# Performance work log

Measured on AMD Instinct MI355X. Metric: run time of the kernel, lower is better.

The kernel has to match this reference:

```python
import jax, jax.numpy as jnp
import numpy as np

DEPTH = 8
DIM = 1024
DI = 2 * DIM        # d_inner (expand=2)
DSTATE = 16         # d_state
DCONV = 4           # conv kernel width
DTRANK = DIM // 16  # dt_rank = ceil(d_model/16) = 64
B = 2
L = 2048
EPS = 1e-5


def setup_inputs() -> dict:
    key = jax.random.key(0)
    ks = jax.random.split(key, 8)
    s = 0.02
    A_log = jnp.broadcast_to(
        jnp.log(jnp.arange(1, DSTATE + 1, dtype=jnp.float32)), (DEPTH, DI, DSTATE)
    )
    return {
        "x": jax.random.normal(ks[0], (B, L, DIM), jnp.float32),
        "in_proj_w": jax.random.normal(ks[1], (DEPTH, 2 * DI, DIM), jnp.float32) * s,
        "conv_w": jax.random.normal(ks[2], (DEPTH, DI, DCONV), jnp.float32) * s,
        "conv_b": jnp.zeros((DEPTH, DI), jnp.float32),
        "x_proj_w": jax.random.normal(ks[3], (DEPTH, DTRANK + 2 * DSTATE, DI), jnp.float32) * s,
        "dt_proj_w": jax.random.normal(ks[4], (DEPTH, DI, DTRANK), jnp.float32) * s,
        "dt_proj_b": jax.random.normal(ks[5], (DEPTH, DI), jnp.float32) * 0.1,
        "A_log": A_log + 0.0,
        "D": jnp.ones((DEPTH, DI), jnp.float32),
        "out_proj_w": jax.random.normal(ks[6], (DEPTH, DIM, DI), jnp.float32) * s,
        "rms_w": jnp.ones((DEPTH, DIM), jnp.float32),
    }


def _selective_scan(xs, delta, Bm, Cm, A):
    # xs, delta: [B, L, DI]; Bm, Cm: [B, L, DSTATE]; A: [DI, DSTATE]
    def step(h, t):
        dt, Bt, Ct, xt = t  # [B,DI], [B,N], [B,N], [B,DI]
        dA = jnp.exp(dt[:, :, None] * A)                      # [B,DI,N]
        h = dA * h + (dt * xt)[:, :, None] * Bt[:, None, :]   # [B,DI,N]
        y = jnp.einsum('bdn,bn->bd', h, Ct)                   # [B,DI]
        return h, y

    h0 = jnp.zeros((xs.shape[0], xs.shape[2], A.shape[1]), xs.dtype)
    ts = (delta.transpose(1, 0, 2), Bm.transpose(1, 0, 2),
          Cm.transpose(1, 0, 2), xs.transpose(1, 0, 2))
    _, ys = jax.lax.scan(step, h0, ts)  # ys: [L,B,DI]
    return ys.transpose(1, 0, 2)


def _mamba(x, Wi, cw, cb, Wx, Wdt, bdt, A_log, Dp, Wo):
    # in_proj (no bias): [B,L,DIM] -> [B,L,2*DI]
    xz = jnp.einsum('bld,ed->ble', x, Wi)
    xs, z = jnp.split(xz, 2, axis=-1)
    # depthwise causal conv1d, kernel DCONV, left pad DCONV-1
    xc = jax.lax.conv_general_dilated(
        xs.transpose(0, 2, 1), cw[:, None, :], (1,), [(DCONV - 1, 0)],
        dimension_numbers=('NCH', 'OIH', 'NCH'), feature_group_count=DI)
    xs = jax.nn.silu(xc + cb[None, :, None]).transpose(0, 2, 1)  # [B,L,DI]
    # x_proj -> dt, B, C
    xdbl = jnp.einsum('bld,ed->ble', xs, Wx)
    dt, Bm, Cm = jnp.split(xdbl, [DTRANK, DTRANK + DSTATE], axis=-1)
    delta = jax.nn.softplus(jnp.einsum('blr,dr->bld', dt, Wdt) + bdt)  # [B,L,DI]
    A = -jnp.exp(A_log)  # [DI, DSTATE]
    y = _selective_scan(xs, delta, Bm, Cm, A) + xs * Dp
    y = y * jax.nn.silu(z)
    return jnp.einsum('bld,ed->ble', y, Wo)  # out_proj, no bias


def _rmsnorm(x, w):
    return x * jax.lax.rsqrt(jnp.mean(x * x, axis=-1, keepdims=True) + EPS) * w


def reference(x, in_proj_w, conv_w, conv_b, x_proj_w, dt_proj_w, dt_proj_b,
              A_log, D, out_proj_w, rms_w):
    for i in range(DEPTH):
        x = _mamba(x, in_proj_w[i], conv_w[i], conv_b[i], x_proj_w[i],
                   dt_proj_w[i], dt_proj_b[i], A_log[i], D[i], out_proj_w[i])
        x = _rmsnorm(x, rms_w[i])
    return x
```

## Files before the change

### kernel.cpp

```cpp
#include <hip/hip_runtime.h>
#include <cstddef>

#define DEPTH  8
#define DIMM   1024
#define DI     2048
#define NST    16
#define DCONVK 4
#define DTRANK 64
#define BB     2
#define LL     2048
#define MM     (BB*LL)
#define BD     (BB*DI)
#define CHK    32
#define LC     (LL/CHK)
#define LOG2E  1.44269504088896f

typedef __attribute__((ext_vector_type(8))) short bf16x8;
typedef __attribute__((ext_vector_type(4))) float f32x4;

__device__ __forceinline__ unsigned short f2bf(float f) {
  unsigned int u = __float_as_uint(f);
  unsigned int r = (u + 0x7fffu + ((u >> 16) & 1u)) >> 16;
  return (unsigned short)r;
}
__device__ __forceinline__ float bf2f(unsigned short h) {
  return __uint_as_float(((unsigned int)h) << 16);
}

__global__ __launch_bounds__(256) void cvt2_k(const float* __restrict__ x,
                                              unsigned short* __restrict__ p,
                                              size_t n) {
  size_t i = ((size_t)blockIdx.x * 256 + threadIdx.x) * 4;
  float4 v = *(const float4*)(x + i);
  float vv[4] = {v.x, v.y, v.z, v.w};
  unsigned short u1[4], u2[4];
#pragma unroll
  for (int k = 0; k < 4; ++k) {
    unsigned short h1 = f2bf(vv[k]);
    u1[k] = h1;
    u2[k] = f2bf(vv[k] - bf2f(h1));
  }
  *(ushort4*)(p + i)     = make_ushort4(u1[0], u1[1], u1[2], u1[3]);
  *(ushort4*)(p + n + i) = make_ushort4(u2[0], u2[1], u2[2], u2[3]);
}

template <int TM>
__global__ __launch_bounds__(256) void gemm_mp(
    const unsigned short* __restrict__ Ap, int lda_a, int pstr_a,
    const unsigned short* __restrict__ Bp, int lda_b, int pstr_b,
    float* __restrict__ C, int M, int N, int K) {
  constexpr int NP    = 2;
  constexpr int NSLOT = NP * (TM + 128) * 4;
  constexpr int ITERS = NSLOT / 256;
  constexpr int NF    = (TM == 128) ? 4 : 2;
  __shared__ unsigned short S[NP * (TM + 128) * 32];

  const int t   = threadIdx.x;
  const int w   = t >> 6;
  const int l   = t & 63;
  const int lm  = l & 15;
  const int q8  = (l >> 4) << 3;
  const int qs  = q8 ^ (((lm >> 1) & 3) << 3);
  const int m0  = blockIdx.y * TM;
  const int n0  = blockIdx.x * 128;
  const int wm  = (TM == 128) ? ((w & 1) << 6) : 0;
  const int wn  = (TM == 128) ? ((w >> 1) << 6) : (w << 5);

  const unsigned short* src[ITERS];
  unsigned short* dst[ITERS];
#pragma unroll
  for (int it = 0; it < ITERS; ++it) {
    int c = it * 256 + t;
    const unsigned short* base;
    int r, aslot;
    if (c < NP * TM * 4) {
      int p  = c / (TM * 4);
      int wi = c % (TM * 4);
      r = wi >> 2; aslot = wi & 3;
      base = Ap + (size_t)p * pstr_a + (size_t)(m0 + r) * lda_a;
    } else {
      int c2 = c - NP * TM * 4;
      int p  = c2 >> 9;
      int wi = c2 & 511;
      r = wi >> 2; aslot = wi & 3;
      base = Bp + (size_t)p * pstr_b + (size_t)(n0 + r) * lda_b;
    }
    int kq = (aslot ^ ((r >> 1) & 3)) << 3;
    src[it] = base + kq;
    dst[it] = &S[(size_t)(it * 256 + (w << 6)) * 8];
  }

  f32x4 acc[4][NF];
#pragma unroll
  for (int i = 0; i < 4; ++i)
#pragma unroll
    for (int j = 0; j < NF; ++j) acc[i][j] = (f32x4){0.f, 0.f, 0.f, 0.f};

  for (int k0 = 0; k0 < K; k0 += 32) {
#pragma unroll
    for (int it = 0; it < ITERS; ++it) {
      __builtin_amdgcn_global_load_lds(
          (const __attribute__((address_space(1))) unsigned int*)src[it],
          (__attribute__((address_space(3))) unsigned int*)dst[it], 16, 0, 0);
      src[it] += 32;
    }
    __syncthreads();
    bf16x8 a0[4], aX[4], b0[NF];
#pragma unroll
    for (int i = 0; i < 4; ++i)
      a0[i] = *(const bf16x8*)&S[(wm + i * 16 + lm) * 32 + qs];
#pragma unroll
    for (int j = 0; j < NF; ++j)
      b0[j] = *(const bf16x8*)&S[NP * TM * 32 + (wn + j * 16 + lm) * 32 + qs];
#pragma unroll
    for (int i = 0; i < 4; ++i)
#pragma unroll
      for (int j = 0; j < NF; ++j)
        acc[i][j] = __builtin_amdgcn_mfma_f32_16x16x32_bf16(a0[i], b0[j], acc[i][j], 0, 0, 0);
#pragma unroll
    for (int j = 0; j < NF; ++j)
      aX[j & 3] = *(const bf16x8*)&S[NP * TM * 32 + 128 * 32 + (wn + j * 16 + lm) * 32 + qs];
#pragma unroll
    for (int i = 0; i < 4; ++i)
#pragma unroll
      for (int j = 0; j < NF; ++j)
        acc[i][j] = __builtin_amdgcn_mfma_f32_16x16x32_bf16(a0[i], aX[j], acc[i][j], 0, 0, 0);
#pragma unroll
    for (int i = 0; i < 4; ++i)
      aX[i] = *(const bf16x8*)&S[TM * 32 + (wm + i * 16 + lm) * 32 + qs];
#pragma unroll
    for (int i = 0; i < 4; ++i)
#pragma unroll
      for (int j = 0; j < NF; ++j)
        acc[i][j] = __builtin_amdgcn_mfma_f32_16x16x32_bf16(aX[i], b0[j], acc[i][j], 0, 0, 0);
    __syncthreads();
  }

  const int row0 = (l >> 4) << 2;
#pragma unroll
  for (int i = 0; i < 4; ++i)
#pragma unroll
    for (int j = 0; j < NF; ++j)
#pragma unroll
      for (int r = 0; r < 4; ++r) {
        int m = m0 + wm + i * 16 + row0 + r;
        int n = n0 + wn + j * 16 + lm;
        C[(size_t)m * N + n] = acc[i][j][r];
      }
}

__global__ __launch_bounds__(256) void dtproj_mp(const unsigned short* __restrict__ Ap,
                                                 const unsigned short* __restrict__ Bp,
                                                 const float* __restrict__ bdt,
                                                 float* __restrict__ Cd) {
  __shared__ unsigned short S[32768];
  const int t  = threadIdx.x;
  const int w  = t >> 6;
  const int l  = t & 63;
  const int lm = l & 15;
  const int q8 = (l >> 4) << 3;
  const int qs = q8 ^ (((lm >> 1) & 3) << 3);
  const int m0 = blockIdx.y * 128;
  const int n0 = blockIdx.x * 128;
  const int wm = (w & 1) << 6;
  const int wn = (w >> 1) << 6;

#pragma unroll
  for (int it = 0; it < 16; ++it) {
    int c  = it * 256 + t;
    int kt = c >> 11;
    int c2 = c & 2047;
    const unsigned short* base;
    int r, aslot;
    if (c2 < 1024) {
      int p = c2 >> 9; int wi = c2 & 511; r = wi >> 2; aslot = wi & 3;
      base = Ap + (size_t)p * (MM * 64) + (size_t)(m0 + r) * 64;
    } else {
      int c3 = c2 - 1024;
      int p = c3 >> 9; int wi = c3 & 511; r = wi >> 2; aslot = wi & 3;
      base = Bp + (size_t)p * (DI * 64) + (size_t)(n0 + r) * 64;
    }
    int kq = (aslot ^ ((r >> 1) & 3)) << 3;
    __builtin_amdgcn_global_load_lds(
        (const __attribute__((address_space(1))) unsigned int*)(base + kt * 32 + kq),
        (__attribute__((address_space(3))) unsigned int*)&S[(size_t)(it * 256 + (w << 6)) * 8],
        16, 0, 0);
  }
  __syncthreads();

  f32x4 acc[4][4];
#pragma unroll
  for (int i = 0; i < 4; ++i)
#pragma unroll
    for (int j = 0; j < 4; ++j) acc[i][j] = (f32x4){0.f, 0.f, 0.f, 0.f};

#pragma unroll
  for (int kt = 0; kt < 2; ++kt) {
    const int RA = kt * 16384;
    const int RB = kt * 16384 + 8192;
    bf16x8 a0[4], aX[4], b0[4];
#pragma unroll
    for (int i = 0; i < 4; ++i)
      a0[i] = *(const bf16x8*)&S[RA + (wm + i * 16 + lm) * 32 + qs];
#pragma unroll
    for (int j = 0; j < 4; ++j)
      b0[j] = *(const bf16x8*)&S[RB + (wn + j * 16 + lm) * 32 + qs];
#pragma unroll
    for (int i = 0; i < 4; ++i)
#pragma unroll
      for (int j = 0; j < 4; ++j)
        acc[i][j] = __builtin_amdgcn_mfma_f32_16x16x32_bf16(a0[i], b0[j], acc[i][j], 0, 0, 0);
#pragma unroll
    for (int j = 0; j < 4; ++j)
      aX[j] = *(const bf16x8*)&S[RB + 4096 + (wn + j * 16 + lm) * 32 + qs];
#pragma unroll
    for (int i = 0; i < 4; ++i)
#pragma unroll
      for (int j = 0; j < 4; ++j)
        acc[i][j] = __builtin_amdgcn_mfma_f32_16x16x32_bf16(a0[i], aX[j], acc[i][j], 0, 0, 0);
#pragma unroll
    for (int i = 0; i < 4; ++i)
      aX[i] = *(const bf16x8*)&S[RA + 4096 + (wm + i * 16 + lm) * 32 + qs];
#pragma unroll
    for (int i = 0; i < 4; ++i)
#pragma unroll
      for (int j = 0; j < 4; ++j)
        acc[i][j] = __builtin_amdgcn_mfma_f32_16x16x32_bf16(aX[i], b0[j], acc[i][j], 0, 0, 0);
  }

  const int row0 = (l >> 4) << 2;
#pragma unroll
  for (int j = 0; j < 4; ++j) {
    int n = n0 + wn + j * 16 + lm;
    float bv = bdt[n];
#pragma unroll
    for (int i = 0; i < 4; ++i)
#pragma unroll
      for (int r = 0; r < 4; ++r) {
        int m = m0 + wm + i * 16 + row0 + r;
        float x = acc[i][j][r] + bv;
        Cd[(size_t)m * DI + n] = fmaxf(x, 0.f) + log1pf(expf(-fabsf(x)));
      }
  }
}

#define XPN 96
__global__ __launch_bounds__(256) void xproj_part_k(const float* __restrict__ A,
                                                    const float* __restrict__ W,
                                                    float* __restrict__ Cp) {
  __shared__ float As[16][128];
  __shared__ float Ws[16][XPN];
  const int t  = threadIdx.x;
  const int tx = t & 15;
  const int ty = t >> 4;
  const int m0 = blockIdx.x * 128;
  const int kb = blockIdx.y * 256;
  float acc[8][6];
#pragma unroll
  for (int i = 0; i < 8; ++i)
#pragma unroll
    for (int j = 0; j < 6; ++j) acc[i][j] = 0.f;

  for (int k0 = kb; k0 < kb + 256; k0 += 16) {
#pragma unroll
    for (int e = t; e < 512; e += 256) {
      int r = e >> 2, cq = (e & 3) << 2;
      float4 v = *(const float4*)(A + (size_t)(m0 + r) * DI + k0 + cq);
      As[cq+0][r] = v.x; As[cq+1][r] = v.y; As[cq+2][r] = v.z; As[cq+3][r] = v.w;
    }
    for (int e = t; e < 384; e += 256) {
      int r = e >> 2, cq = (e & 3) << 2;
      float4 v = *(const float4*)(W + (size_t)r * DI + k0 + cq);
      Ws[cq+0][r] = v.x; Ws[cq+1][r] = v.y; Ws[cq+2][r] = v.z; Ws[cq+3][r] = v.w;
    }
    __syncthreads();
#pragma unroll
    for (int kk = 0; kk < 16; ++kk) {
      float a[8], b[6];
#pragma unroll
      for (int i = 0; i < 8; ++i) a[i] = As[kk][ty*8 + i];
#pragma unroll
      for (int j = 0; j < 6; ++j) b[j] = Ws[kk][tx*6 + j];
#pragma unroll
      for (int i = 0; i < 8; ++i)
#pragma unroll
        for (int j = 0; j < 6; ++j) acc[i][j] += a[i] * b[j];
    }
    __syncthreads();
  }
  float* cp = Cp + (size_t)blockIdx.y * MM * XPN;
#pragma unroll
  for (int i = 0; i < 8; ++i)
#pragma unroll
    for (int j = 0; j < 6; ++j)
      cp[(size_t)(m0 + ty*8 + i) * XPN + tx*6 + j] = acc[i][j];
}

__global__ __launch_bounds__(256) void xproj_red_k(const float* __restrict__ Cp,
                                                   float* __restrict__ o,
                                                   unsigned short* __restrict__ dtp) {
  int i = blockIdx.x * 256 + threadIdx.x;
  float s = 0.f;
#pragma unroll
  for (int ks = 0; ks < 8; ++ks) s += Cp[(size_t)ks * (MM * XPN) + i];
  o[i] = s;
  int m = i / 96, col = i - m * 96;
  if (col < DTRANK) {
    unsigned short h1 = f2bf(s);
    dtp[(size_t)m * DTRANK + col] = h1;
    dtp[(size_t)MM * DTRANK + (size_t)m * DTRANK + col] = f2bf(s - bf2f(h1));
  }
}

__device__ __forceinline__ float fast_silu(float x) {
  return x * __builtin_amdgcn_rcpf(1.f + exp2f(-LOG2E * x));
}

__global__ __launch_bounds__(256) void conv_silu_k(const float* __restrict__ xz,
                                                   const float* __restrict__ cw,
                                                   const float* __restrict__ cb,
                                                   float* __restrict__ xc) {
  int idx = blockIdx.x * 256 + threadIdx.x;
  int c  = idx & (DI - 1);
  int bl = idx >> 11;
  int l  = bl & (LL - 1);
  float acc = cb[c];
#pragma unroll
  for (int k = 0; k < DCONVK; ++k) {
    int ls = l - (DCONVK - 1) + k;
    if (ls >= 0)
      acc += xz[(size_t)(bl - (DCONVK - 1) + k) * (2*DI) + c] * cw[c*DCONVK + k];
  }
  xc[idx] = fast_silu(acc);
}

__global__ __launch_bounds__(256) void scan_pass1(const float* __restrict__ delta,
                                                  const float* __restrict__ xc,
                                                  const float* __restrict__ xdbl,
                                                  const float* __restrict__ A_log,
                                                  float* __restrict__ Hc,
                                                  float* __restrict__ Sdt) {
  const int t  = threadIdx.x;
  const int c  = blockIdx.x >> 6;
  const int g  = blockIdx.x & 63;
  const int q  = t >> 2;
  const int nq = t & 3;
  const int ch = g * 64 + q;
  const int b  = ch >> 11;
  const int d  = ch & (DI - 1);
  const size_t rowbase = (size_t)b * LL + (size_t)c * LC;

  __shared__ float Bs[LC * 16];
  { int row = t >> 2, seg = t & 3;
    *(float4*)&Bs[row * 16 + seg * 4] =
        *(const float4*)(xdbl + (rowbase + row) * 96 + DTRANK + seg * 4);
  }
  __syncthreads();

  float4 al = *(const float4*)(A_log + (size_t)d * NST + nq * 4);
  const float Av0 = -expf(al.x) * LOG2E, Av1 = -expf(al.y) * LOG2E;
  const float Av2_ = -expf(al.z) * LOG2E, Av3 = -expf(al.w) * LOG2E;
  float h0 = 0.f, h1 = 0.f, h2 = 0.f, h3 = 0.f, S = 0.f;

#define P1_SU 4
  float aD[P1_SU], aX[P1_SU];
  float bD[P1_SU], bX[P1_SU];

#define P1_LOAD(l0, D_, X_)                                            \
  { _Pragma("unroll")                                                  \
    for (int u = 0; u < P1_SU; ++u) {                                  \
      size_t bl = rowbase + (l0) + u;                                  \
      D_[u] = delta[bl * DI + d];                                      \
      X_[u] = xc[bl * DI + d];                                         \
    } }

#define P1_COMP(l0, D_, X_)                                            \
  { _Pragma("unroll")                                                  \
    for (int u = 0; u < P1_SU; ++u) {                                  \
      float4 Bv = *(const float4*)&Bs[((l0) + u) * 16 + nq * 4];       \
      float dt = D_[u], uB = dt * X_[u];                               \
      h0 = fmaf(exp2f(dt * Av0), h0, uB * Bv.x);                       \
      h1 = fmaf(exp2f(dt * Av1), h1, uB * Bv.y);                       \
      h2 = fmaf(exp2f(dt * Av2_), h2, uB * Bv.z);                      \
      h3 = fmaf(exp2f(dt * Av3), h3, uB * Bv.w);                       \
      S += dt;                                                         \
    } }

  P1_LOAD(0, aD, aX);
  for (int l0 = 0; l0 < LC; l0 += 2 * P1_SU) {
    P1_LOAD(l0 + P1_SU, bD, bX);
    P1_COMP(l0, aD, aX);
    if (l0 + 2 * P1_SU < LC) P1_LOAD(l0 + 2 * P1_SU, aD, aX);
    P1_COMP(l0 + P1_SU, bD, bX);
  }
#undef P1_LOAD
#undef P1_COMP
  size_t hi = ((size_t)c * BD + ch) * NST + nq * 4;
  float4 hv; hv.x = h0; hv.y = h1; hv.z = h2; hv.w = h3;
  *(float4*)(Hc + hi) = hv;
  if (nq == 0) Sdt[(size_t)c * BD + ch] = S;
}

__global__ __launch_bounds__(256) void scan_pass2(float* __restrict__ Hc,
                                                  const float* __restrict__ Sdt,
                                                  const float* __restrict__ A_log) {
  const int g  = blockIdx.x * 256 + threadIdx.x;
  const int n  = g & (NST - 1);
  const int ch = g >> 4;
  const int d  = ch & (DI - 1);
  const float Av2 = -expf(A_log[d * NST + n]) * LOG2E;
  float Sv[CHK];
#pragma unroll
  for (int c = 0; c < CHK; ++c) Sv[c] = Sdt[(size_t)c * BD + ch];
  float h = 0.f;
  float tmp = Hc[(size_t)ch * NST + n];
#pragma unroll
  for (int c = 0; c < CHK; ++c) {
    size_t idx = ((size_t)c * BD + ch) * NST + n;
    float tnext = (c + 1 < CHK) ? Hc[((size_t)(c+1) * BD + ch) * NST + n] : 0.f;
    Hc[idx] = h;
    h = fmaf(exp2f(Av2 * Sv[c]), h, tmp);
    tmp = tnext;
  }
}

__global__ __launch_bounds__(256) void scan_pass3(const float* __restrict__ delta,
                                                  const float* __restrict__ xc,
                                                  const float* __restrict__ xdbl,
                                                  const float* __restrict__ A_log,
                                                  float* __restrict__ xzp,
                                                  const float* __restrict__ Dp,
                                                  const float* __restrict__ Hc) {
  const int t  = threadIdx.x;
  const int c  = blockIdx.x >> 6;
  const int g  = blockIdx.x & 63;
  const int q  = t >> 2;
  const int nq = t & 3;
  const int ch = g * 64 + q;
  const int b  = ch >> 11;
  const int d  = ch & (DI - 1);
  const size_t rowbase = (size_t)b * LL + (size_t)c * LC;

  __shared__ float BCs[LC * 32];
  {
#pragma unroll
    for (int e = t; e < 512; e += 256) {
      int row = e >> 3, seg = e & 7;
      *(float4*)&BCs[row * 32 + seg * 4] =
          *(const float4*)(xdbl + (rowbase + row) * 96 + DTRANK + seg * 4);
    }
  }
  __syncthreads();

  float4 al = *(const float4*)(A_log + (size_t)d * NST + nq * 4);
  const float Av0 = -expf(al.x) * LOG2E, Av1 = -expf(al.y) * LOG2E;
  const float Av2_ = -expf(al.z) * LOG2E, Av3 = -expf(al.w) * LOG2E;
  const float Dv = Dp[d];
  float4 hv = *(const float4*)(Hc + ((size_t)c * BD + ch) * NST + nq * 4);
  float h0 = hv.x, h1 = hv.y, h2 = hv.z, h3 = hv.w;
  unsigned short* yp = (unsigned short*)xzp;

#define P3_SU 2
  float aD[P3_SU], aX[P3_SU], aZ[P3_SU];
  float bD[P3_SU], bX[P3_SU], bZ[P3_SU];

#define P3_LOAD(l0, D_, X_, Z_)                                        \
  { _Pragma("unroll")                                                  \
    for (int u = 0; u < P3_SU; ++u) {                                  \
      size_t bl = rowbase + (l0) + u;                                  \
      D_[u] = delta[bl * DI + d];                                      \
      X_[u] = xc[bl * DI + d];                                         \
      Z_[u] = xzp[bl * (2*DI) + DI + d];                               \
    } }

#define P3_COMP(l0, D_, X_, Z_)                                        \
  { _Pragma("unroll")                                                  \
    for (int u = 0; u < P3_SU; ++u) {                                  \
      float4 Bv = *(const float4*)&BCs[((l0) + u) * 32 + nq * 4];      \
      float4 Cv = *(const float4*)&BCs[((l0) + u) * 32 + 16 + nq * 4]; \
      float dt = D_[u], uB = dt * X_[u];                               \
      h0 = fmaf(exp2f(dt * Av0), h0, uB * Bv.x);                       \
      h1 = fmaf(exp2f(dt * Av1), h1, uB * Bv.y);                       \
      h2 = fmaf(exp2f(dt * Av2_), h2, uB * Bv.z);                      \
      h3 = fmaf(exp2f(dt * Av3), h3, uB * Bv.w);                       \
      float s = fmaf(h1, Cv.y, h0 * Cv.x);                             \
      float t2 = fmaf(h3, Cv.w, h2 * Cv.z);                            \
      s += t2;                                                         \
      s += __shfl_xor(s, 1, 4);                                        \
      s += __shfl_xor(s, 2, 4);                                        \
      if (nq == 0) {                                                   \
        float yv = (s + X_[u] * Dv) * fast_silu(Z_[u]);                \
        unsigned short y1 = f2bf(yv);                                  \
        unsigned short y2 = f2bf(yv - bf2f(y1));                       \
        size_t bl = rowbase + (l0) + u;                                \
        yp[bl * 8192 + d] = y1;                                        \
        yp[bl * 8192 + 2048 + d] = y2;                                 \
      }                                                                \
    } }

  P3_LOAD(0, aD, aX, aZ);
  for (int l0 = 0; l0 < LC; l0 += 2 * P3_SU) {
    P3_LOAD(l0 + P3_SU, bD, bX, bZ);
    P3_COMP(l0, aD, aX, aZ);
    if (l0 + 2 * P3_SU < LC) P3_LOAD(l0 + 2 * P3_SU, aD, aX, aZ);
    P3_COMP(l0 + P3_SU, bD, bX, bZ);
  }
#undef P3_LOAD
#undef P3_COMP
}

template <bool PLANES>
__global__ __launch_bounds__(256) void rmsnorm_k(const float* __restrict__ x,
                                                 const float* __restrict__ w,
                                                 float* __restrict__ o,
                                                 unsigned short* __restrict__ op) {
  int row = blockIdx.x;
  const float* xr = x + (size_t)row * DIMM;
  float s = 0.f;
  for (int i = threadIdx.x; i < DIMM; i += 256) { float v = xr[i]; s += v * v; }
#pragma unroll
  for (int off = 32; off > 0; off >>= 1) s += __shfl_xor(s, off, 64);
  __shared__ float red[4];
  if ((threadIdx.x & 63) == 0) red[threadIdx.x >> 6] = s;
  __syncthreads();
  float tot = red[0] + red[1] + red[2] + red[3];
  float scale = rsqrtf(tot * (1.0f / DIMM) + 1e-5f);
  for (int i = threadIdx.x; i < DIMM; i += 256) {
    float v = xr[i] * scale * w[i];
    if (PLANES) {
      unsigned short h1 = f2bf(v);
      op[(size_t)row * DIMM + i] = h1;
      op[(size_t)MM * DIMM + (size_t)row * DIMM + i] = f2bf(v - bf2f(h1));
    } else {
      o[(size_t)row * DIMM + i] = v;
    }
  }
}

extern "C" void kernel_launch(void* const* d_in, const int* in_sizes, int n_in,
                              void* d_out, int out_size, void* d_ws, size_t ws_size,
                              hipStream_t stream) {
  (void)in_sizes; (void)n_in; (void)out_size; (void)ws_size;
  const float* x_in    = (const float*)d_in[0];
  const float* Wi_all  = (const float*)d_in[1];
  const float* cw_all  = (const float*)d_in[2];
  const float* cb_all  = (const float*)d_in[3];
  const float* Wx_all  = (const float*)d_in[4];
  const float* Wdt_all = (const float*)d_in[5];
  const float* bdt_all = (const float*)d_in[6];
  const float* Alog_all= (const float*)d_in[7];
  const float* D_all   = (const float*)d_in[8];
  const float* Wo_all  = (const float*)d_in[9];
  const float* rw_all  = (const float*)d_in[10];
  float* out = (float*)d_out;

  float* ws    = (float*)d_ws;
  float* xz    = ws;
  float* xc    = xz   + (size_t)MM * 2 * DI;
  float* xdbl  = xc   + (size_t)MM * DI;
  float* delta = xdbl + (size_t)MM * 96;
  float* xbuf  = delta+ (size_t)MM * DI;
  float* outtmp = xc;

  unsigned short* xpl  = (unsigned short*)delta;
  unsigned short* wipl = (unsigned short*)xc;
  unsigned short* wopl = (unsigned short*)(xc + (size_t)4194304);
  float*          Cp   = delta;
  float* Hc   = xbuf;
  float* Sdt  = Hc + (size_t)CHK * BD * NST;
  unsigned short* dtpl  = (unsigned short*)(xbuf + 2228224);
  unsigned short* wdtpl = (unsigned short*)(xbuf + 2490368);

  const int EW_GRID = (MM * DI) / 256;
  const int SCAN_GRID = CHK * 64;

  for (int i = 0; i < DEPTH; ++i) {
    const float* Wi   = Wi_all  + (size_t)i * (2*DI) * DIMM;
    const float* cw   = cw_all  + (size_t)i * DI * DCONVK;
    const float* cb   = cb_all  + (size_t)i * DI;
    const float* Wx   = Wx_all  + (size_t)i * 96 * DI;
    const float* Wdt  = Wdt_all + (size_t)i * DI * DTRANK;
    const float* bdt  = bdt_all + (size_t)i * DI;
    const float* Alog = Alog_all+ (size_t)i * DI * NST;
    const float* Dp   = D_all   + (size_t)i * DI;
    const float* Wo   = Wo_all  + (size_t)i * DIMM * DI;
    const float* rw   = rw_all  + (size_t)i * DIMM;

    if (i == 0)
      cvt2_k<<<(MM*DIMM)/1024, 256, 0, stream>>>(x_in, xpl, (size_t)MM * DIMM);
    cvt2_k<<<((2*DI)*DIMM)/1024, 256, 0, stream>>>(Wi, wipl, (size_t)(2*DI) * DIMM);
    gemm_mp<128><<<dim3((2*DI)/128, MM/128), 256, 0, stream>>>(
        xpl, DIMM, MM*DIMM, wipl, DIMM, (2*DI)*DIMM, xz, MM, 2*DI, DIMM);
    conv_silu_k<<<EW_GRID, 256, 0, stream>>>(xz, cw, cb, xc);
    xproj_part_k<<<dim3(MM/128, 8), 256, 0, stream>>>(xc, Wx, Cp);
    xproj_red_k<<<(MM*XPN)/256, 256, 0, stream>>>(Cp, xdbl, dtpl);
    cvt2_k<<<(DI*DTRANK)/1024, 256, 0, stream>>>(Wdt, wdtpl, (size_t)DI * DTRANK);
    dtproj_mp<<<dim3(DI/128, MM/128), 256, 0, stream>>>(dtpl, wdtpl, bdt, delta);
    scan_pass1<<<SCAN_GRID, 256, 0, stream>>>(delta, xc, xdbl, Alog, Hc, Sdt);
    scan_pass2<<<(BD*NST)/256, 256, 0, stream>>>(Hc, Sdt, Alog);
    scan_pass3<<<SCAN_GRID, 256, 0, stream>>>(delta, xc, xdbl, Alog, xz, Dp, Hc);
    cvt2_k<<<(DIMM*DI)/1024, 256, 0, stream>>>(Wo, wopl, (size_t)DIMM * DI);
    gemm_mp<64><<<dim3(DIMM/128, MM/64), 256, 0, stream>>>(
        (const unsigned short*)xz, 8192, 2048, wopl, DI, DIMM*DI,
        outtmp, MM, DIMM, DI);
    if (i < DEPTH - 1)
      rmsnorm_k<true><<<MM, 256, 0, stream>>>(outtmp, rw, nullptr, xpl);
    else
      rmsnorm_k<false><<<MM, 256, 0, stream>>>(outtmp, rw, out, nullptr);
  }
}
```

Before: 3.663 ms.

## Add 256x256-tile in_proj GEMM with async LDS loads and split-phase pipelining

```diff
diff --git a/kernel.cpp b/kernel.cpp
--- a/kernel.cpp
+++ b/kernel.cpp
@@ -141,6 +141,129 @@
   for (int i = 0; i < 4; ++i)
 #pragma unroll
     for (int j = 0; j < NF; ++j)
+#pragma unroll
+      for (int r = 0; r < 4; ++r) {
+        int m = m0 + wm + i * 16 + row0 + r;
+        int n = n0 + wn + j * 16 + lm;
+        C[(size_t)m * N + n] = acc[i][j][r];
+      }
+}
+
+__global__ __launch_bounds__(512) void gemm256_mp(
+    const unsigned short* __restrict__ Ap, int lda_a, int pstr_a,
+    const unsigned short* __restrict__ Bp, int lda_b, int pstr_b,
+    float* __restrict__ C, int M, int N, int K) {
+  __shared__ unsigned short S[65536];
+  const int t  = threadIdx.x;
+  const int w  = t >> 6;
+  const int l  = t & 63;
+  const int lm = l & 15;
+  const int qs = ((l >> 4) << 3) ^ (((lm >> 1) & 3) << 3);
+  const int m0 = blockIdx.y * 256;
+  const int n0 = blockIdx.x * 256;
+  const int wm = (w & 1) << 7;
+  const int wn = (w >> 1) << 6;
+
+  const int rr = t >> 2;
+  const int kq = ((t & 3) ^ ((rr >> 1) & 3)) << 3;
+  const unsigned short* srcA = Ap + (size_t)(m0 + rr) * lda_a + kq;
+  const unsigned short* srcB = Bp + (size_t)(n0 + rr) * lda_b + kq;
+  const size_t a128 = (size_t)128 * lda_a;
+  const size_t b128 = (size_t)128 * lda_b;
+  const int dbase = (w << 6) * 8;
+
+#define G256_ISSUE(p_, it_)                                                    \
+  __builtin_amdgcn_global_load_lds(                                            \
+      (const __attribute__((address_space(1))) unsigned int*)(p_),             \
+      (__attribute__((address_space(3))) unsigned int*)&S[bnext + (it_)*4096 + dbase], \
+      16, 0, 0)
+
+  f32x4 acc[8][4];
+#pragma unroll
+  for (int i = 0; i < 8; ++i)
+#pragma unroll
+    for (int j = 0; j < 4; ++j) acc[i][j] = (f32x4){0.f, 0.f, 0.f, 0.f};
+
+  {
+    const int bnext = 0;
+    const size_t kb = 0;
+    G256_ISSUE(srcA + kb, 0);          G256_ISSUE(srcA + a128 + kb, 1);
+    G256_ISSUE(srcB + kb, 4);          G256_ISSUE(srcB + b128 + kb, 5);
+    G256_ISSUE(srcB + pstr_b + kb, 6); G256_ISSUE(srcB + pstr_b + b128 + kb, 7);
+    G256_ISSUE(srcA + pstr_a + kb, 2); G256_ISSUE(srcA + pstr_a + a128 + kb, 3);
+  }
+  asm volatile("s_waitcnt vmcnt(4)" ::: "memory");
+  __builtin_amdgcn_s_barrier();
+
+  const int NT = K >> 5;
+#pragma unroll 2
+  for (int ti = 0; ti < NT; ++ti) {
+    const int bcur  = (ti & 1) << 15;
+    const int bnext = bcur ^ 32768;
+    const int kkt   = (ti + 1 < NT) ? (ti + 1) : 0;
+    const size_t kb = (size_t)kkt * 32;
+    const unsigned short* Sb = &S[bcur];
+    bf16x8 a[8], b0[4], b1[4];
+
+#pragma unroll
+    for (int i = 0; i < 8; ++i)
+      a[i] = *(const bf16x8*)&Sb[(wm + i * 16 + lm) * 32 + qs];
+#pragma unroll
+    for (int j = 0; j < 4; ++j)
+      b0[j] = *(const bf16x8*)&Sb[16384 + (wn + j * 16 + lm) * 32 + qs];
+    G256_ISSUE(srcA + kb, 0); G256_ISSUE(srcA + a128 + kb, 1);
+    G256_ISSUE(srcB + kb, 4); G256_ISSUE(srcB + b128 + kb, 5);
+    asm volatile("s_waitcnt vmcnt(6)" ::: "memory");
+    __builtin_amdgcn_s_barrier();
+    asm volatile("s_waitcnt lgkmcnt(0)" ::: "memory");
+    __builtin_amdgcn_s_setprio(1);
+#pragma unroll
+    for (int i = 0; i < 8; ++i)
+#pragma unroll
+      for (int j = 0; j < 4; ++j)
+        acc[i][j] = __builtin_amdgcn_mfma_f32_16x16x32_bf16(a[i], b0[j], acc[i][j], 0, 0, 0);
+    __builtin_amdgcn_s_setprio(0);
+    __builtin_amdgcn_s_barrier();
+
+#pragma unroll
+    for (int j = 0; j < 4; ++j)
+      b1[j] = *(const bf16x8*)&Sb[24576 + (wn + j * 16 + lm) * 32 + qs];
+    G256_ISSUE(srcB + pstr_b + kb, 6); G256_ISSUE(srcB + pstr_b + b128 + kb, 7);
+    asm volatile("s_waitcnt vmcnt(6)" ::: "memory");
+    __builtin_amdgcn_s_barrier();
+    asm volatile("s_waitcnt lgkmcnt(0)" ::: "memory");
+    __builtin_amdgcn_s_setprio(1);
+#pragma unroll
+    for (int i = 0; i < 8; ++i)
+#pragma unroll
+      for (int j = 0; j < 4; ++j)
+        acc[i][j] = __builtin_amdgcn_mfma_f32_16x16x32_bf16(a[i], b1[j], acc[i][j], 0, 0, 0);
+    __builtin_amdgcn_s_setprio(0);
+    __builtin_amdgcn_s_barrier();
+
+#pragma unroll
+    for (int i = 0; i < 8; ++i)
+      a[i] = *(const bf16x8*)&Sb[8192 + (wm + i * 16 + lm) * 32 + qs];
+    G256_ISSUE(srcA + pstr_a + kb, 2); G256_ISSUE(srcA + pstr_a + a128 + kb, 3);
+    asm volatile("s_waitcnt vmcnt(4)" ::: "memory");
+    __builtin_amdgcn_s_barrier();
+    asm volatile("s_waitcnt lgkmcnt(0)" ::: "memory");
+    __builtin_amdgcn_s_setprio(1);
+#pragma unroll
+    for (int i = 0; i < 8; ++i)
+#pragma unroll
+      for (int j = 0; j < 4; ++j)
+        acc[i][j] = __builtin_amdgcn_mfma_f32_16x16x32_bf16(a[i], b0[j], acc[i][j], 0, 0, 0);
+    __builtin_amdgcn_s_setprio(0);
+    __builtin_amdgcn_s_barrier();
+  }
+#undef G256_ISSUE
+
+  const int row0 = (l >> 4) << 2;
+#pragma unroll
+  for (int i = 0; i < 8; ++i)
+#pragma unroll
+    for (int j = 0; j < 4; ++j)
 #pragma unroll
       for (int r = 0; r < 4; ++r) {
         int m = m0 + wm + i * 16 + row0 + r;
@@ -589,7 +712,7 @@
     if (i == 0)
       cvt2_k<<<(MM*DIMM)/1024, 256, 0, stream>>>(x_in, xpl, (size_t)MM * DIMM);
     cvt2_k<<<((2*DI)*DIMM)/1024, 256, 0, stream>>>(Wi, wipl, (size_t)(2*DI) * DIMM);
-    gemm_mp<128><<<dim3((2*DI)/128, MM/128), 256, 0, stream>>>(
+    gemm256_mp<<<dim3((2*DI)/256, MM/256), 512, 0, stream>>>(
         xpl, DIMM, MM*DIMM, wipl, DIMM, (2*DI)*DIMM, xz, MM, 2*DI, DIMM);
     conv_silu_k<<<EW_GRID, 256, 0, stream>>>(xz, cw, cb, xc);
     xproj_part_k<<<dim3(MM/128, 8), 256, 0, stream>>>(xc, Wx, Cp);
```

New measurement: 3.356 ms. -8.4%, faster.

## Replace split-bf16 GEMM with 256-row double-buffered two-phase kernel and split-K out_proj

Applied to the files above, without the earlier changes.

```diff
diff --git a/kernel.cpp b/kernel.cpp
--- a/kernel.cpp
+++ b/kernel.cpp
@@ -44,108 +44,145 @@
   *(ushort4*)(p + n + i) = make_ushort4(u2[0], u2[1], u2[2], u2[3]);
 }
 
-template <int TM>
-__global__ __launch_bounds__(256) void gemm_mp(
+template <int BN, int NSPLIT>
+__global__ __launch_bounds__(512, 2) void gemm2ph(
     const unsigned short* __restrict__ Ap, int lda_a, int pstr_a,
     const unsigned short* __restrict__ Bp, int lda_b, int pstr_b,
-    float* __restrict__ C, int M, int N, int K) {
-  constexpr int NP    = 2;
-  constexpr int NSLOT = NP * (TM + 128) * 4;
-  constexpr int ITERS = NSLOT / 256;
-  constexpr int NF    = (TM == 128) ? 4 : 2;
-  __shared__ unsigned short S[NP * (TM + 128) * 32];
-
-  const int t   = threadIdx.x;
-  const int w   = t >> 6;
-  const int l   = t & 63;
-  const int lm  = l & 15;
-  const int q8  = (l >> 4) << 3;
-  const int qs  = q8 ^ (((lm >> 1) & 3) << 3);
-  const int m0  = blockIdx.y * TM;
-  const int n0  = blockIdx.x * 128;
-  const int wm  = (TM == 128) ? ((w & 1) << 6) : 0;
-  const int wn  = (TM == 128) ? ((w >> 1) << 6) : (w << 5);
-
-  const unsigned short* src[ITERS];
-  unsigned short* dst[ITERS];
-#pragma unroll
-  for (int it = 0; it < ITERS; ++it) {
-    int c = it * 256 + t;
-    const unsigned short* base;
-    int r, aslot;
-    if (c < NP * TM * 4) {
-      int p  = c / (TM * 4);
-      int wi = c % (TM * 4);
-      r = wi >> 2; aslot = wi & 3;
-      base = Ap + (size_t)p * pstr_a + (size_t)(m0 + r) * lda_a;
-    } else {
-      int c2 = c - NP * TM * 4;
-      int p  = c2 >> 9;
-      int wi = c2 & 511;
-      r = wi >> 2; aslot = wi & 3;
-      base = Bp + (size_t)p * pstr_b + (size_t)(n0 + r) * lda_b;
-    }
-    int kq = (aslot ^ ((r >> 1) & 3)) << 3;
-    src[it] = base + kq;
-    dst[it] = &S[(size_t)(it * 256 + (w << 6)) * 8];
-  }
-
-  f32x4 acc[4][NF];
-#pragma unroll
-  for (int i = 0; i < 4; ++i)
-#pragma unroll
-    for (int j = 0; j < NF; ++j) acc[i][j] = (f32x4){0.f, 0.f, 0.f, 0.f};
-
-  for (int k0 = 0; k0 < K; k0 += 32) {
-#pragma unroll
-    for (int it = 0; it < ITERS; ++it) {
-      __builtin_amdgcn_global_load_lds(
-          (const __attribute__((address_space(1))) unsigned int*)src[it],
-          (__attribute__((address_space(3))) unsigned int*)dst[it], 16, 0, 0);
-      src[it] += 32;
-    }
-    __syncthreads();
-    bf16x8 a0[4], aX[4], b0[NF];
-#pragma unroll
-    for (int i = 0; i < 4; ++i)
-      a0[i] = *(const bf16x8*)&S[(wm + i * 16 + lm) * 32 + qs];
-#pragma unroll
-    for (int j = 0; j < NF; ++j)
-      b0[j] = *(const bf16x8*)&S[NP * TM * 32 + (wn + j * 16 + lm) * 32 + qs];
-#pragma unroll
-    for (int i = 0; i < 4; ++i)
-#pragma unroll
-      for (int j = 0; j < NF; ++j)
-        acc[i][j] = __builtin_amdgcn_mfma_f32_16x16x32_bf16(a0[i], b0[j], acc[i][j], 0, 0, 0);
-#pragma unroll
-    for (int j = 0; j < NF; ++j)
-      aX[j & 3] = *(const bf16x8*)&S[NP * TM * 32 + 128 * 32 + (wn + j * 16 + lm) * 32 + qs];
-#pragma unroll
-    for (int i = 0; i < 4; ++i)
-#pragma unroll
-      for (int j = 0; j < NF; ++j)
-        acc[i][j] = __builtin_amdgcn_mfma_f32_16x16x32_bf16(a0[i], aX[j], acc[i][j], 0, 0, 0);
-#pragma unroll
-    for (int i = 0; i < 4; ++i)
-      aX[i] = *(const bf16x8*)&S[TM * 32 + (wm + i * 16 + lm) * 32 + qs];
-#pragma unroll
-    for (int i = 0; i < 4; ++i)
-#pragma unroll
-      for (int j = 0; j < NF; ++j)
-        acc[i][j] = __builtin_amdgcn_mfma_f32_16x16x32_bf16(aX[i], b0[j], acc[i][j], 0, 0, 0);
-    __syncthreads();
-  }
-
+    float* __restrict__ C0, float* __restrict__ C1, int N, int Ktot) {
+  constexpr int BM  = 256;
+  constexpr int BF  = BN / 64;
+  constexpr int BL  = BN / 128;
+  constexpr int RA1 = BM * 32;
+  constexpr int RB0 = 2 * BM * 32;
+  constexpr int RB1 = 2 * BM * 32 + BN * 32;
+  constexpr int BUFS = (2 * BM + 2 * BN) * 32;
+  __shared__ unsigned short S[2 * BUFS];
+
+  const int t  = threadIdx.x;
+  const int w  = t >> 6;
+  const int l  = t & 63;
+  const int lm = l & 15;
+  const int qs = ((l >> 4) << 3) ^ (((lm >> 1) & 3) << 3);
+
+  const int nx   = gridDim.x;
+  const int nwg  = nx * gridDim.y;
+  const int flat = blockIdx.y * nx + blockIdx.x;
+  const int swz  = (flat & 7) * (nwg >> 3) + (flat >> 3);
+  const int m0 = (swz / nx) * BM;
+  const int n0 = (swz % nx) * BN;
+  const int z  = (NSPLIT == 2) ? blockIdx.z : 0;
+  const int KS = Ktot / NSPLIT;
+
+  const int wm = (w & 1) << 7;
+  const int wn = (w >> 1) * (BN / 4);
+
+  const int rr = t >> 2;
+  const int kq = ((t & 3) ^ ((rr >> 1) & 3)) << 3;
+  const unsigned short* srcA = Ap + (size_t)(m0 + rr) * lda_a + (size_t)z * KS + kq;
+  const unsigned short* srcB = Bp + (size_t)(n0 + rr) * lda_b + (size_t)z * KS + kq;
+  const size_t a128 = (size_t)128 * lda_a;
+  const size_t b128 = (size_t)128 * lda_b;
+  const int dbase = (w << 6) * 8;
+
+#define GI(p_, off_)                                                           \
+  __builtin_amdgcn_global_load_lds(                                            \
+      (const __attribute__((address_space(1))) unsigned int*)(p_),             \
+      (__attribute__((address_space(3))) unsigned int*)&S[bnext + (off_) + dbase], \
+      16, 0, 0)
+
+#define GI_PH0(kb_)                                                            \
+  { GI(srcA + (kb_), 0); GI(srcA + a128 + (kb_), 4096);                        \
+    GI(srcB + (kb_), RB0);                                                     \
+    if (BL == 2) GI(srcB + b128 + (kb_), RB0 + 4096);                          \
+    GI(srcB + (size_t)pstr_b + (kb_), RB1);                                    \
+    if (BL == 2) GI(srcB + (size_t)pstr_b + b128 + (kb_), RB1 + 4096); }
+
+#define GI_PH1(kb_)                                                            \
+  { GI(srcA + (size_t)pstr_a + (kb_), RA1);                                    \
+    GI(srcA + (size_t)pstr_a + a128 + (kb_), RA1 + 4096); }
+
+  f32x4 acc[8][BF];
+#pragma unroll
+  for (int i = 0; i < 8; ++i)
+#pragma unroll
+    for (int j = 0; j < BF; ++j) acc[i][j] = (f32x4){0.f, 0.f, 0.f, 0.f};
+
+  {
+    const int bnext = 0;
+    GI_PH0((size_t)0);
+    GI_PH1((size_t)0);
+  }
+  asm volatile("s_waitcnt vmcnt(2)" ::: "memory");
+  __builtin_amdgcn_s_barrier();
+
+  const int NT = KS >> 5;
+#pragma unroll 2
+  for (int ti = 0; ti < NT; ++ti) {
+    const int bcur  = (ti & 1) ? BUFS : 0;
+    const int bnext = (ti & 1) ? 0 : BUFS;
+    const size_t kb = (size_t)((ti + 1 < NT) ? (ti + 1) : 0) * 32;
+    const unsigned short* Sb = &S[bcur];
+    bf16x8 a[8], b0[BF], b1[BF];
+
+#pragma unroll
+    for (int i = 0; i < 8; ++i)
+      a[i] = *(const bf16x8*)&Sb[(wm + i * 16 + lm) * 32 + qs];
+#pragma unroll
+    for (int j = 0; j < BF; ++j)
+      b0[j] = *(const bf16x8*)&Sb[RB0 + (wn + j * 16 + lm) * 32 + qs];
+#pragma unroll
+    for (int j = 0; j < BF; ++j)
+      b1[j] = *(const bf16x8*)&Sb[RB1 + (wn + j * 16 + lm) * 32 + qs];
+    GI_PH0(kb);
+    if constexpr (BN == 256) asm volatile("s_waitcnt vmcnt(6)" ::: "memory");
+    else                     asm volatile("s_waitcnt vmcnt(4)" ::: "memory");
+    __builtin_amdgcn_s_barrier();
+    asm volatile("s_waitcnt lgkmcnt(0)" ::: "memory");
+    __builtin_amdgcn_s_setprio(1);
+#pragma unroll
+    for (int i = 0; i < 8; ++i)
+#pragma unroll
+      for (int j = 0; j < BF; ++j)
+        acc[i][j] = __builtin_amdgcn_mfma_f32_16x16x32_bf16(a[i], b0[j], acc[i][j], 0, 0, 0);
+#pragma unroll
+    for (int i = 0; i < 8; ++i)
+#pragma unroll
+      for (int j = 0; j < BF; ++j)
+        acc[i][j] = __builtin_amdgcn_mfma_f32_16x16x32_bf16(a[i], b1[j], acc[i][j], 0, 0, 0);
+    __builtin_amdgcn_s_setprio(0);
+    __builtin_amdgcn_s_barrier();
+
+#pragma unroll
+    for (int i = 0; i < 8; ++i)
+      a[i] = *(const bf16x8*)&Sb[RA1 + (wm + i * 16 + lm) * 32 + qs];
+    GI_PH1(kb);
+    asm volatile("s_waitcnt vmcnt(2)" ::: "memory");
+    __builtin_amdgcn_s_barrier();
+    asm volatile("s_waitcnt lgkmcnt(0)" ::: "memory");
+    __builtin_amdgcn_s_setprio(1);
+#pragma unroll
+    for (int i = 0; i < 8; ++i)
+#pragma unroll
+      for (int j = 0; j < BF; ++j)
+        acc[i][j] = __builtin_amdgcn_mfma_f32_16x16x32_bf16(a[i], b0[j], acc[i][j], 0, 0, 0);
+    __builtin_amdgcn_s_setprio(0);
+    __builtin_amdgcn_s_barrier();
+  }
+#undef GI_PH1
+#undef GI_PH0
+#undef GI
+
+  float* Cc = (NSPLIT == 2 && blockIdx.z) ? C1 : C0;
   const int row0 = (l >> 4) << 2;
 #pragma unroll
-  for (int i = 0; i < 4; ++i)
-#pragma unroll
-    for (int j = 0; j < NF; ++j)
+  for (int i = 0; i < 8; ++i)
+#pragma unroll
+    for (int j = 0; j < BF; ++j)
 #pragma unroll
       for (int r = 0; r < 4; ++r) {
         int m = m0 + wm + i * 16 + row0 + r;
         int n = n0 + wn + j * 16 + lm;
-        C[(size_t)m * N + n] = acc[i][j][r];
+        Cc[(size_t)m * N + n] = acc[i][j][r];
       }
 }
 
@@ -511,13 +548,17 @@
 
 template <bool PLANES>
 __global__ __launch_bounds__(256) void rmsnorm_k(const float* __restrict__ x,
+                                                 const float* __restrict__ x2,
                                                  const float* __restrict__ w,
                                                  float* __restrict__ o,
                                                  unsigned short* __restrict__ op) {
   int row = blockIdx.x;
-  const float* xr = x + (size_t)row * DIMM;
+  const float* xr  = x  + (size_t)row * DIMM;
+  const float* x2r = x2 + (size_t)row * DIMM;
   float s = 0.f;
-  for (int i = threadIdx.x; i < DIMM; i += 256) { float v = xr[i]; s += v * v; }
+  for (int i = threadIdx.x; i < DIMM; i += 256) {
+    float v = xr[i] + x2r[i]; s += v * v;
+  }
 #pragma unroll
   for (int off = 32; off > 0; off >>= 1) s += __shfl_xor(s, off, 64);
   __shared__ float red[4];
@@ -526,7 +567,7 @@
   float tot = red[0] + red[1] + red[2] + red[3];
   float scale = rsqrtf(tot * (1.0f / DIMM) + 1e-5f);
   for (int i = threadIdx.x; i < DIMM; i += 256) {
-    float v = xr[i] * scale * w[i];
+    float v = (xr[i] + x2r[i]) * scale * w[i];
     if (PLANES) {
       unsigned short h1 = f2bf(v);
       op[(size_t)row * DIMM + i] = h1;
@@ -566,6 +607,7 @@
   unsigned short* wipl = (unsigned short*)xc;
   unsigned short* wopl = (unsigned short*)(xc + (size_t)4194304);
   float*          Cp   = delta;
+  float* part1 = delta + (size_t)4194304;
   float* Hc   = xbuf;
   float* Sdt  = Hc + (size_t)CHK * BD * NST;
   unsigned short* dtpl  = (unsigned short*)(xbuf + 2228224);
@@ -589,8 +631,8 @@
     if (i == 0)
       cvt2_k<<<(MM*DIMM)/1024, 256, 0, stream>>>(x_in, xpl, (size_t)MM * DIMM);
     cvt2_k<<<((2*DI)*DIMM)/1024, 256, 0, stream>>>(Wi, wipl, (size_t)(2*DI) * DIMM);
-    gemm_mp<128><<<dim3((2*DI)/128, MM/128), 256, 0, stream>>>(
-        xpl, DIMM, MM*DIMM, wipl, DIMM, (2*DI)*DIMM, xz, MM, 2*DI, DIMM);
+    gemm2ph<256,1><<<dim3((2*DI)/256, MM/256, 1), 512, 0, stream>>>(
+        xpl, DIMM, MM*DIMM, wipl, DIMM, (2*DI)*DIMM, xz, nullptr, 2*DI, DIMM);
     conv_silu_k<<<EW_GRID, 256, 0, stream>>>(xz, cw, cb, xc);
     xproj_part_k<<<dim3(MM/128, 8), 256, 0, stream>>>(xc, Wx, Cp);
     xproj_red_k<<<(MM*XPN)/256, 256, 0, stream>>>(Cp, xdbl, dtpl);
@@ -600,12 +642,12 @@
     scan_pass2<<<(BD*NST)/256, 256, 0, stream>>>(Hc, Sdt, Alog);
     scan_pass3<<<SCAN_GRID, 256, 0, stream>>>(delta, xc, xdbl, Alog, xz, Dp, Hc);
     cvt2_k<<<(DIMM*DI)/1024, 256, 0, stream>>>(Wo, wopl, (size_t)DIMM * DI);
-    gemm_mp<64><<<dim3(DIMM/128, MM/64), 256, 0, stream>>>(
+    gemm2ph<128,2><<<dim3(DIMM/128, MM/256, 2), 512, 0, stream>>>(
         (const unsigned short*)xz, 8192, 2048, wopl, DI, DIMM*DI,
-        outtmp, MM, DIMM, DI);
+        outtmp, part1, DIMM, DI);
     if (i < DEPTH - 1)
-      rmsnorm_k<true><<<MM, 256, 0, stream>>>(outtmp, rw, nullptr, xpl);
+      rmsnorm_k<true><<<MM, 256, 0, stream>>>(outtmp, part1, rw, nullptr, xpl);
     else
-      rmsnorm_k<false><<<MM, 256, 0, stream>>>(outtmp, rw, out, nullptr);
-  }
-}
+      rmsnorm_k<false><<<MM, 256, 0, stream>>>(outtmp, part1, rw, out, nullptr);
+  }
+}
```

Result: faster. 3.259 ms (-11.0%).
